# Performance work log

Measured on AMD Instinct MI355X. Metric: run time of the kernel, lower is better.

Reference implementation:

```python
import jax, jax.numpy as jnp
import numpy as np

N = 50000      # num nodes
E = 800000     # num edges (avg degree 16)
H = 128        # hidden_dim
D = 3          # node_dim (decoder output)
L = 4          # num_layers


def setup_inputs() -> dict:
    key = jax.random.key(0)
    ks = jax.random.split(key, 6)
    s = 0.05
    x = jax.random.normal(ks[0], (N, H), dtype=jnp.float32)
    edge_index = jax.random.randint(ks[1], (2, E), 0, N, dtype=jnp.int64)
    # per-layer EdgeConv MLP params: Linear(2H->H), ReLU, Linear(H->H)
    W1 = jax.random.normal(ks[2], (L, 2 * H, H), dtype=jnp.float32) * s
    b1 = jnp.zeros((L, H), dtype=jnp.float32)
    W2 = jax.random.normal(ks[3], (L, H, H), dtype=jnp.float32) * s
    b2 = jnp.zeros((L, H), dtype=jnp.float32)
    # final fc: Linear(H -> D)
    Wf = jax.random.normal(ks[4], (H, D), dtype=jnp.float32) * s
    bf = jnp.zeros((D,), dtype=jnp.float32)
    return {"x": x, "edge_index": edge_index, "W1": W1, "b1": b1,
            "W2": W2, "b2": b2, "Wf": Wf, "bf": bf}


def reference(x, edge_index, W1, b1, W2, b2, Wf, bf):
    n = x.shape[0]
    # add_self_loops: every node has at least one incoming message
    loops = jnp.arange(n, dtype=edge_index.dtype)
    src = jnp.concatenate([edge_index[0], loops])  # x_j source
    dst = jnp.concatenate([edge_index[1], loops])  # x_i target / aggregate index
    for l in range(W1.shape[0]):
        x_i = x[dst]                                   # [E+N, H] gather targets
        x_j = x[src]                                   # [E+N, H] gather sources
        msg = jnp.concatenate([x_i, x_j - x_i], axis=-1)   # [E+N, 2H]
        msg = jax.nn.relu(msg @ W1[l] + b1[l]) @ W2[l] + b2[l]  # edge MLP
        x = jax.ops.segment_max(msg, dst, num_segments=n)       # max aggregate
    return x @ Wf + bf  # [N, D]
```

## Files before the change

### kernel.cpp

```cpp
#include <hip/hip_runtime.h>
#include <hip/hip_fp16.h>

typedef _Float16 f16;
typedef _Float16 f16x8 __attribute__((ext_vector_type(8)));
typedef __fp16 hf16x2 __attribute__((ext_vector_type(2)));
typedef float f32x4 __attribute__((ext_vector_type(4)));
typedef float f32x2 __attribute__((ext_vector_type(2)));
typedef unsigned int u32;
typedef u32 u32x4 __attribute__((ext_vector_type(4)));

#define HDIM 128
#define LAYERS 4
#define TS 48
#define NEG_BIG (-3.0e38f)

static __device__ __forceinline__ f32x4 mfma16(f16x8 a, f16x8 b, f32x4 c) {
  return __builtin_amdgcn_mfma_f32_16x16x32_f16(a, b, c, 0, 0, 0);
}

static __device__ __forceinline__ void atomicMaxF(float* addr, float val) {
  if (val >= 0.f) atomicMax((int*)addr, __float_as_int(val));
  else            atomicMin((unsigned int*)addr, __float_as_uint(val));
}

static __device__ __forceinline__ f16x8 pack4(hf16x2 a, hf16x2 b, hf16x2 c, hf16x2 d) {
  u32x4 u = {__builtin_bit_cast(u32, a), __builtin_bit_cast(u32, b),
             __builtin_bit_cast(u32, c), __builtin_bit_cast(u32, d)};
  return __builtin_bit_cast(f16x8, u);
}

static __device__ __forceinline__ void split8(f32x4 a, f32x4 b, f16x8& hv, f16x8& lv) {
  hf16x2 h0 = __builtin_amdgcn_cvt_pkrtz(a.x, a.y);
  hf16x2 h1 = __builtin_amdgcn_cvt_pkrtz(a.z, a.w);
  hf16x2 h2 = __builtin_amdgcn_cvt_pkrtz(b.x, b.y);
  hf16x2 h3 = __builtin_amdgcn_cvt_pkrtz(b.z, b.w);
  hv = pack4(h0, h1, h2, h3);
  hf16x2 l0 = __builtin_amdgcn_cvt_pkrtz(a.x - (float)h0[0], a.y - (float)h0[1]);
  hf16x2 l1 = __builtin_amdgcn_cvt_pkrtz(a.z - (float)h1[0], a.w - (float)h1[1]);
  hf16x2 l2 = __builtin_amdgcn_cvt_pkrtz(b.x - (float)h2[0], b.y - (float)h2[1]);
  hf16x2 l3 = __builtin_amdgcn_cvt_pkrtz(b.z - (float)h3[0], b.w - (float)h3[1]);
  lv = pack4(l0, l1, l2, l3);
}

__global__ void gnn_hist(const int* __restrict__ ei, int* __restrict__ deg, int E) {
  int e = blockIdx.x * 256 + threadIdx.x;
  if (e < E) atomicAdd(&deg[ei[E + e]], 1);
}

__global__ void gnn_bsum(const int* __restrict__ deg, int* __restrict__ bsum, int N) {
  __shared__ int red[256];
  int v = blockIdx.x * 256 + threadIdx.x;
  red[threadIdx.x] = (v < N) ? (deg[v] + 1) : 0;
  __syncthreads();
  for (int d = 128; d; d >>= 1) {
    if (threadIdx.x < d) red[threadIdx.x] += red[threadIdx.x + d];
    __syncthreads();
  }
  if (threadIdx.x == 0) bsum[blockIdx.x] = red[0];
}

__global__ void gnn_bscan(const int* __restrict__ bsum, int* __restrict__ boffs,
                          int* __restrict__ offs, int nb, int N) {
  __shared__ int sh[256];
  int t = threadIdx.x;
  sh[t] = (t < nb) ? bsum[t] : 0;
  __syncthreads();
  for (int d = 1; d < 256; d <<= 1) {
    int add = (t >= d) ? sh[t - d] : 0;
    __syncthreads();
    sh[t] += add;
    __syncthreads();
  }
  boffs[t] = (t > 0) ? sh[t - 1] : 0;
  if (t == 255) offs[N] = sh[255];
}

__global__ void gnn_scan_fin(const int* __restrict__ deg, const int* __restrict__ boffs,
                             int* __restrict__ offs, int* __restrict__ cursor,
                             int* __restrict__ colsrc, int* __restrict__ nodeof, int N) {
  __shared__ int sh[256];
  int t = threadIdx.x;
  int v = blockIdx.x * 256 + t;
  int val = (v < N) ? (deg[v] + 1) : 0;
  sh[t] = val;
  __syncthreads();
  for (int d = 1; d < 256; d <<= 1) {
    int add = (t >= d) ? sh[t - d] : 0;
    __syncthreads();
    sh[t] += add;
    __syncthreads();
  }
  if (v < N) {
    int excl = boffs[blockIdx.x] + sh[t] - val;
    offs[v] = excl;
    cursor[v] = excl + 1;
    colsrc[excl] = v;
    int e = excl + val;
    for (int s = excl; s < e; s++) nodeof[s] = v;
  }
}

__global__ void gnn_scatter(const int* __restrict__ ei, int* __restrict__ cursor,
                            int* __restrict__ colsrc, int E) {
  int e = blockIdx.x * 256 + threadIdx.x;
  if (e < E) {
    int d = ei[E + e];
    int p = atomicAdd(&cursor[d], 1);
    colsrc[p] = ei[e];
  }
}

__global__ void gnn_biasprep(const float* __restrict__ W1, const float* __restrict__ b1,
                             const float* __restrict__ b2, const float* __restrict__ Wf,
                             const float* __restrict__ bf, float* __restrict__ cbias,
                             float* __restrict__ bfp) {
  int l = blockIdx.x, c = threadIdx.x;
  if (l < LAYERS) {
    float s = 0.f;
    if (l > 0) {
      const float* bp = b2 + (size_t)(l - 1) * HDIM;
      if (c < 128) {
        for (int k = 0; k < 128; k++)
          s += bp[k] * (W1[((size_t)l * 256 + k) * 128 + c] - W1[((size_t)l * 256 + 128 + k) * 128 + c]);
      } else {
        int cc = c - 128;
        for (int k = 0; k < 128; k++)
          s += bp[k] * W1[((size_t)l * 256 + 128 + k) * 128 + cc];
      }
    }
    float base = (c < 128) ? b1[(size_t)l * HDIM + c] : 0.f;
    cbias[l * 256 + c] = base + s;
  } else if (c < 3) {
    float s = bf[c];
    for (int k = 0; k < 128; k++) s += b2[3 * HDIM + k] * Wf[k * 3 + c];
    bfp[c] = s;
  }
}

__global__ void gnn_wprep1(const float* __restrict__ W1, f16* __restrict__ Wc) {
  int id = blockIdx.x * 256 + threadIdx.x;
  if (id >= LAYERS * 128 * 256) return;
  int col = id & 255, k = (id >> 8) & 127, l = id >> 15;
  float w;
  if (col < 128) w = W1[((size_t)l * 256 + k) * 128 + col] - W1[((size_t)l * 256 + 128 + k) * 128 + col];
  else           w = W1[((size_t)l * 256 + 128 + k) * 128 + (col - 128)];
  f16 hi = (f16)w;
  f16 lo = (f16)(w - (float)hi);
  int kk = k >> 5, quad = (k >> 3) & 3, j = k & 7;
  int ntile = col >> 4, lane = quad * 16 + (col & 15);
  size_t base = ((((size_t)l * 2 + 0) * 4 + kk) * 16 + ntile) * 512 + lane * 8 + j;
  Wc[base] = hi;
  Wc[base + (size_t)4 * 16 * 512] = lo;
}

__global__ void gnn_wprep2(const float* __restrict__ W2, f16* __restrict__ W2f) {
  int id = blockIdx.x * 256 + threadIdx.x;
  if (id >= LAYERS * 128 * 128) return;
  int n = id & 127, k = (id >> 7) & 127, l = id >> 14;
  float w = W2[((size_t)l * 128 + k) * 128 + n];
  f16 hi = (f16)w;
  f16 lo = (f16)(w - (float)hi);
  int kk = k >> 5, quad = (k >> 3) & 3, j = k & 7;
  int ntile = n >> 4, lane = quad * 16 + (n & 15);
  size_t base = ((((size_t)l * 2 + 0) * 4 + kk) * 8 + ntile) * 512 + lane * 8 + j;
  W2f[base] = hi;
  W2f[base + (size_t)4 * 8 * 512] = lo;
}

__global__ __launch_bounds__(256) void gnn_pq(const float* __restrict__ x,
    const f16* __restrict__ Wc, const float* __restrict__ cbias,
    float* __restrict__ P, float* __restrict__ Q, int N,
    const int* __restrict__ offs, int spb, float* __restrict__ xinit) {
  __shared__ __align__(16) f16 shA[2 * 4 * 4 * 64 * 8];
  int tid = threadIdx.x;
  int row0 = blockIdx.x * 64;
#pragma unroll
  for (int i = 0; i < 4; i++) {
    int p = i * 256 + tid;
    int row = p & 63, seg = p >> 6;
    f32x4 a = {}, b = {};
    int gr = row0 + row;
    if (gr < N) {
      const f32x4* xp = (const f32x4*)(x + (size_t)gr * HDIM + seg * 8);
      a = xp[0]; b = xp[1];
    }
    f16x8 hv, lv;
    split8(a, b, hv, lv);
    int kk = seg >> 2, quad = seg & 3, mt = row >> 4, m = row & 15;
    int lane = quad * 16 + m;
    int off = ((kk * 4 + mt) * 64 + lane) * 8;
    *(f16x8*)&shA[off] = hv;
    *(f16x8*)&shA[off + 4 * 4 * 64 * 8] = lv;
  }
  __syncthreads();
  int wave = tid >> 6, lane = tid & 63;
  int quad = lane >> 4, cl = lane & 15;
  f16x8 bw[2][4][4];
#pragma unroll
  for (int pl = 0; pl < 2; pl++)
#pragma unroll
    for (int nt = 0; nt < 4; nt++)
#pragma unroll
      for (int kk = 0; kk < 4; kk++) {
        int ntile = wave * 4 + nt;
        bw[pl][nt][kk] = *(const f16x8*)&Wc[(((size_t)(pl * 4 + kk) * 16 + ntile) * 64 + lane) * 8];
      }
#pragma unroll
  for (int mt = 0; mt < 4; mt++) {
    f32x4 acc[4] = {};
#pragma unroll
    for (int kk = 0; kk < 4; kk++) {
      f16x8 ah = *(const f16x8*)&shA[((kk * 4 + mt) * 64 + lane) * 8];
      f16x8 al = *(const f16x8*)&shA[(((4 + kk) * 4 + mt) * 64 + lane) * 8];
#pragma unroll
      for (int nt = 0; nt < 4; nt++) {
        acc[nt] = mfma16(ah, bw[0][nt][kk], acc[nt]);
        acc[nt] = mfma16(al, bw[0][nt][kk], acc[nt]);
        acc[nt] = mfma16(ah, bw[1][nt][kk], acc[nt]);
      }
    }
#pragma unroll
    for (int nt = 0; nt < 4; nt++) {
      int c = (wave * 4 + nt) * 16 + cl;
      float bb = cbias[c];
      float* dst = (c < HDIM) ? P : Q;
      int cc = c & 127;
#pragma unroll
      for (int i = 0; i < 4; i++) {
        int gr = row0 + mt * 16 + quad * 4 + i;
        if (gr < N) dst[(size_t)gr * HDIM + cc] = acc[nt][i] + bb;
      }
    }
  }
  if (tid < 64) {
    int v = row0 + tid;
    if (v < N) {
      int a = offs[v], b = offs[v + 1] - 1;
      if (a / spb != b / spb) {
        f32x4 ninf = {NEG_BIG, NEG_BIG, NEG_BIG, NEG_BIG};
        float* xr = xinit + (size_t)v * HDIM;
#pragma unroll
        for (int c = 0; c < HDIM; c += 4) *(f32x4*)(xr + c) = ninf;
      }
    }
  }
}

__global__ __launch_bounds__(256, 3) void gnn_edge4(
    const float* __restrict__ P, const float* __restrict__ Q,
    const int* __restrict__ offs, const int* __restrict__ colsrc,
    const int* __restrict__ nodeof, const f16* __restrict__ W2f,
    float* __restrict__ xout, int S, int spb) {
  __shared__ __align__(16) f16 shA[2 * 4 * 3 * 64 * 8];
  __shared__ __align__(16) float msg[TS * 132];
  __shared__ __align__(16) float stradV[2][128];
  __shared__ int stradN[2];
  int tid = threadIdx.x;
  int wave = tid >> 6, lane = tid & 63;
  int quad = lane >> 4, cl = lane & 15;
  f16x8 bw[2][2][4];
#pragma unroll
  for (int pl = 0; pl < 2; pl++)
#pragma unroll
    for (int nt = 0; nt < 2; nt++)
#pragma unroll
      for (int kk = 0; kk < 4; kk++)
        bw[pl][nt][kk] = *(const f16x8*)&W2f[(((size_t)(pl * 4 + kk) * 8 + (wave * 2 + nt)) * 64 + lane) * 8];
  int blk0 = blockIdx.x * spb;
  int blk1 = blk0 + spb; if (blk1 > S) blk1 = S;
  if (tid < 2) stradN[tid] = -1;
  int sl = tid >> 4, seg = tid & 15;
  int kkb = seg >> 2, qb = seg & 3;
  int laneF = qb * 16 + sl;
  int tc = 0;
  for (int t0 = blk0; t0 < blk1; t0 += TS, tc++) {
    int par = tc & 1, prv = par ^ 1;
    int tEnd = t0 + TS; if (tEnd > blk1) tEnd = blk1;
#pragma unroll
    for (int i = 0; i < 3; i++) {
      int slot = t0 + i * 16 + sl;
      int slc = (slot < S) ? slot : (S - 1);
      int src = colsrc[slc];
      int dst = nodeof[slc];
      const f32x4* qp = (const f32x4*)(Q + (size_t)src * HDIM + seg * 8);
      const f32x4* pp = (const f32x4*)(P + (size_t)dst * HDIM + seg * 8);
      f32x4 qa = qp[0], qb4 = qp[1], pa = pp[0], pb = pp[1];
      f32x4 sa, sb;
      sa.x = fmaxf(pa.x + qa.x, 0.f); sa.y = fmaxf(pa.y + qa.y, 0.f);
      sa.z = fmaxf(pa.z + qa.z, 0.f); sa.w = fmaxf(pa.w + qa.w, 0.f);
      sb.x = fmaxf(pb.x + qb4.x, 0.f); sb.y = fmaxf(pb.y + qb4.y, 0.f);
      sb.z = fmaxf(pb.z + qb4.z, 0.f); sb.w = fmaxf(pb.w + qb4.w, 0.f);
      f16x8 hv, lv;
      split8(sa, sb, hv, lv);
      int off = ((kkb * 3 + i) * 64 + laneF) * 8;
      *(f16x8*)&shA[off] = hv;
      *(f16x8*)&shA[off + 6144] = lv;
    }
    __syncthreads();
    if (tid == 0) stradN[par] = -1;
    f32x4 acc[3][2] = {};
#pragma unroll
    for (int kk = 0; kk < 4; kk++)
#pragma unroll
      for (int mt = 0; mt < 3; mt++) {
        int off = ((kk * 3 + mt) * 64 + lane) * 8;
        f16x8 ah = *(const f16x8*)&shA[off];
        f16x8 al = *(const f16x8*)&shA[off + 6144];
#pragma unroll
        for (int nt = 0; nt < 2; nt++) {
          acc[mt][nt] = mfma16(ah, bw[0][nt][kk], acc[mt][nt]);
          acc[mt][nt] = mfma16(al, bw[0][nt][kk], acc[mt][nt]);
          acc[mt][nt] = mfma16(ah, bw[1][nt][kk], acc[mt][nt]);
        }
      }
#pragma unroll
    for (int mt = 0; mt < 3; mt++)
#pragma unroll
      for (int nt = 0; nt < 2; nt++) {
        int col = wave * 32 + nt * 16 + cl;
#pragma unroll
        for (int i = 0; i < 4; i++) {
          int row = mt * 16 + quad * 4 + i;
          msg[row * 132 + col] = acc[mt][nt][i];
        }
      }
    __syncthreads();
    int vA = nodeof[t0];
    int vB = nodeof[tEnd - 1];
    int sNp = stradN[prv];
    int ngroups = (vB - vA + 1) << 5;
    for (int p = tid; p < ngroups; p += 256) {
      int v = vA + (p >> 5), c4 = (p & 31) << 2;
      int a = offs[v], b = offs[v + 1];
      int r0 = (a > t0 ? a : t0) - t0;
      int r1 = (b < tEnd ? b : tEnd) - t0;
      f32x4 m = {NEG_BIG, NEG_BIG, NEG_BIG, NEG_BIG};
      for (int r = r0; r < r1; r++) {
        f32x4 x = *(const f32x4*)&msg[r * 132 + c4];
        m.x = fmaxf(m.x, x.x); m.y = fmaxf(m.y, x.y);
        m.z = fmaxf(m.z, x.z); m.w = fmaxf(m.w, x.w);
      }
      if (v == sNp) {
        f32x4 sv = *(const f32x4*)&stradV[prv][c4];
        m.x = fmaxf(m.x, sv.x); m.y = fmaxf(m.y, sv.y);
        m.z = fmaxf(m.z, sv.z); m.w = fmaxf(m.w, sv.w);
      }
      if (b > tEnd && tEnd < blk1) {
        *(f32x4*)&stradV[par][c4] = m;
        if ((p & 31) == 0) stradN[par] = v;
      } else {
        float* dp = &xout[(size_t)v * HDIM + c4];
        if (a < blk0 || b > blk1) {
          atomicMaxF(dp + 0, m.x); atomicMaxF(dp + 1, m.y);
          atomicMaxF(dp + 2, m.z); atomicMaxF(dp + 3, m.w);
        } else {
          *(f32x4*)dp = m;
        }
      }
    }
  }
}

__global__ __launch_bounds__(256) void gnn_fc(const float* __restrict__ x,
    const float* __restrict__ Wf, const float* __restrict__ bfp,
    float* __restrict__ out, int N) {
  int wave = threadIdx.x >> 6, lane = threadIdx.x & 63;
  int wid = blockIdx.x * 4 + wave, nw = gridDim.x * 4;
  int k0 = lane * 2;
  float w00 = Wf[k0 * 3 + 0], w01 = Wf[k0 * 3 + 1], w02 = Wf[k0 * 3 + 2];
  float w10 = Wf[k0 * 3 + 3], w11 = Wf[k0 * 3 + 4], w12 = Wf[k0 * 3 + 5];
  float bf0 = bfp[0], bf1 = bfp[1], bf2 = bfp[2];
  for (int v = wid; v < N; v += nw) {
    f32x2 xx = *(const f32x2*)(x + (size_t)v * HDIM + k0);
    float d0 = xx.x * w00 + xx.y * w10;
    float d1 = xx.x * w01 + xx.y * w11;
    float d2 = xx.x * w02 + xx.y * w12;
#pragma unroll
    for (int s = 32; s; s >>= 1) {
      d0 += __shfl_xor(d0, s, 64);
      d1 += __shfl_xor(d1, s, 64);
      d2 += __shfl_xor(d2, s, 64);
    }
    if (lane == 0) {
      out[(size_t)v * 3 + 0] = d0 + bf0;
      out[(size_t)v * 3 + 1] = d1 + bf1;
      out[(size_t)v * 3 + 2] = d2 + bf2;
    }
  }
}

extern "C" void kernel_launch(void* const* d_in, const int* in_sizes, int n_in,
                              void* d_out, int out_size, void* d_ws, size_t ws_size,
                              hipStream_t stream) {
  const float* x_in = (const float*)d_in[0];
  const int*   ei   = (const int*)d_in[1];
  const float* W1   = (const float*)d_in[2];
  const float* b1   = (const float*)d_in[3];
  const float* W2   = (const float*)d_in[4];
  const float* b2   = (const float*)d_in[5];
  const float* Wf   = (const float*)d_in[6];
  const float* bfv  = (const float*)d_in[7];
  float* outp = (float*)d_out;
  int N = in_sizes[0] / HDIM;
  int E = in_sizes[1] / 2;
  int S = E + N;

  char* ws = (char*)d_ws;
  size_t o = 0;
  auto alloc = [&](size_t bytes) -> char* {
    char* p = ws + o;
    o += (bytes + 255) & ~(size_t)255;
    return p;
  };
  int*   deg    = (int*)alloc((size_t)N * 4);
  int*   offs   = (int*)alloc(((size_t)N + 1) * 4);
  int*   cursor = (int*)alloc((size_t)N * 4);
  int*   colsrc = (int*)alloc((size_t)S * 4);
  int*   nodeof = (int*)alloc((size_t)S * 4);
  int*   bsum   = (int*)alloc(256 * 4);
  int*   boffs  = (int*)alloc(256 * 4);
  float* cbias  = (float*)alloc((size_t)LAYERS * 256 * 4);
  float* bfp    = (float*)alloc(4 * 4);
  float* P      = (float*)alloc((size_t)N * HDIM * 4);
  float* Q      = (float*)alloc((size_t)N * HDIM * 4);
  float* xbuf   = (float*)alloc((size_t)N * HDIM * 4);
  f16*   Wc     = (f16*)alloc((size_t)LAYERS * 65536 * 2);
  f16*   W2f    = (f16*)alloc((size_t)LAYERS * 32768 * 2);
  (void)ws_size; (void)n_in; (void)out_size;

  int nb = (N + 255) / 256;
  hipMemsetAsync(deg, 0, (size_t)N * 4, stream);
  gnn_hist<<<(E + 255) / 256, 256, 0, stream>>>(ei, deg, E);
  gnn_bsum<<<nb, 256, 0, stream>>>(deg, bsum, N);
  gnn_bscan<<<1, 256, 0, stream>>>(bsum, boffs, offs, nb, N);
  gnn_scan_fin<<<nb, 256, 0, stream>>>(deg, boffs, offs, cursor, colsrc, nodeof, N);
  gnn_scatter<<<(E + 255) / 256, 256, 0, stream>>>(ei, cursor, colsrc, E);
  gnn_biasprep<<<LAYERS + 1, 256, 0, stream>>>(W1, b1, b2, Wf, bfv, cbias, bfp);
  gnn_wprep1<<<(LAYERS * 128 * 256 + 255) / 256, 256, 0, stream>>>(W1, Wc);
  gnn_wprep2<<<(LAYERS * 128 * 128 + 255) / 256, 256, 0, stream>>>(W2, W2f);

  int spb = ((((S + 1023) / 1024) + TS - 1) / TS) * TS;
  int NB = (S + spb - 1) / spb;
  const float* xc = x_in;
  for (int l = 0; l < LAYERS; l++) {
    gnn_pq<<<(N + 63) / 64, 256, 0, stream>>>(xc, Wc + (size_t)l * 65536, cbias + l * 256,
                                              P, Q, N, offs, spb, xbuf);
    gnn_edge4<<<NB, 256, 0, stream>>>(P, Q, offs, colsrc, nodeof, W2f + (size_t)l * 32768,
                                      xbuf, S, spb);
    xc = xbuf;
  }
  gnn_fc<<<256, 256, 0, stream>>>(xc, Wf, bfp, outp, N);
}
```

Before: 926.7 us.

## Software-prefetch next edge tile's P/Q gathers and shrink tile to 32

The edge kernel now loads the P/Q rows for the next tile into registers while the current tile's MFMA work runs, and prefetches colsrc/nodeof indices two tiles ahead. The tile size drops from 48 to 32 edge slots and occupancy is raised to 4 blocks per CU, which shrinks shared memory and accumulator use. The goal is to hide gather latency. In exchange, the extra prefetch registers raise register pressure, and the smaller tiles mean more loop iterations and barriers per slot.

```diff
diff --git a/kernel.cpp b/kernel.cpp
--- a/kernel.cpp
+++ b/kernel.cpp
@@ -11,7 +11,7 @@
 
 #define HDIM 128
 #define LAYERS 4
-#define TS 48
+#define TS 32
 #define NEG_BIG (-3.0e38f)
 
 static __device__ __forceinline__ f32x4 mfma16(f16x8 a, f16x8 b, f32x4 c) {
@@ -246,12 +246,12 @@
   }
 }
 
-__global__ __launch_bounds__(256, 3) void gnn_edge4(
+__global__ __launch_bounds__(256, 4) void gnn_edge5(
     const float* __restrict__ P, const float* __restrict__ Q,
     const int* __restrict__ offs, const int* __restrict__ colsrc,
     const int* __restrict__ nodeof, const f16* __restrict__ W2f,
     float* __restrict__ xout, int S, int spb) {
-  __shared__ __align__(16) f16 shA[2 * 4 * 3 * 64 * 8];
+  __shared__ __align__(16) f16 shA[2 * 4 * 2 * 64 * 8];
   __shared__ __align__(16) float msg[TS * 132];
   __shared__ __align__(16) float stradV[2][128];
   __shared__ int stradN[2];
@@ -272,40 +272,69 @@
   int sl = tid >> 4, seg = tid & 15;
   int kkb = seg >> 2, qb = seg & 3;
   int laneF = qb * 16 + sl;
+  int Sm1 = S - 1;
+
+  int cs[2], nd[2];
+  f32x4 qv[2][2], pv[2][2];
+#pragma unroll
+  for (int i = 0; i < 2; i++) {
+    int slc = blk0 + i * 16 + sl; slc = (slc < S) ? slc : Sm1;
+    cs[i] = colsrc[slc]; nd[i] = nodeof[slc];
+  }
+#pragma unroll
+  for (int i = 0; i < 2; i++) {
+    const f32x4* qp = (const f32x4*)(Q + (size_t)cs[i] * HDIM + seg * 8);
+    const f32x4* pp = (const f32x4*)(P + (size_t)nd[i] * HDIM + seg * 8);
+    qv[i][0] = qp[0]; qv[i][1] = qp[1];
+    pv[i][0] = pp[0]; pv[i][1] = pp[1];
+  }
+#pragma unroll
+  for (int i = 0; i < 2; i++) {
+    int slc = blk0 + TS + i * 16 + sl; slc = (slc < S) ? slc : Sm1;
+    cs[i] = colsrc[slc]; nd[i] = nodeof[slc];
+  }
+
   int tc = 0;
   for (int t0 = blk0; t0 < blk1; t0 += TS, tc++) {
     int par = tc & 1, prv = par ^ 1;
     int tEnd = t0 + TS; if (tEnd > blk1) tEnd = blk1;
 #pragma unroll
-    for (int i = 0; i < 3; i++) {
-      int slot = t0 + i * 16 + sl;
-      int slc = (slot < S) ? slot : (S - 1);
-      int src = colsrc[slc];
-      int dst = nodeof[slc];
-      const f32x4* qp = (const f32x4*)(Q + (size_t)src * HDIM + seg * 8);
-      const f32x4* pp = (const f32x4*)(P + (size_t)dst * HDIM + seg * 8);
-      f32x4 qa = qp[0], qb4 = qp[1], pa = pp[0], pb = pp[1];
+    for (int i = 0; i < 2; i++) {
       f32x4 sa, sb;
-      sa.x = fmaxf(pa.x + qa.x, 0.f); sa.y = fmaxf(pa.y + qa.y, 0.f);
-      sa.z = fmaxf(pa.z + qa.z, 0.f); sa.w = fmaxf(pa.w + qa.w, 0.f);
-      sb.x = fmaxf(pb.x + qb4.x, 0.f); sb.y = fmaxf(pb.y + qb4.y, 0.f);
-      sb.z = fmaxf(pb.z + qb4.z, 0.f); sb.w = fmaxf(pb.w + qb4.w, 0.f);
+      sa.x = fmaxf(pv[i][0].x + qv[i][0].x, 0.f); sa.y = fmaxf(pv[i][0].y + qv[i][0].y, 0.f);
+      sa.z = fmaxf(pv[i][0].z + qv[i][0].z, 0.f); sa.w = fmaxf(pv[i][0].w + qv[i][0].w, 0.f);
+      sb.x = fmaxf(pv[i][1].x + qv[i][1].x, 0.f); sb.y = fmaxf(pv[i][1].y + qv[i][1].y, 0.f);
+      sb.z = fmaxf(pv[i][1].z + qv[i][1].z, 0.f); sb.w = fmaxf(pv[i][1].w + qv[i][1].w, 0.f);
       f16x8 hv, lv;
       split8(sa, sb, hv, lv);
-      int off = ((kkb * 3 + i) * 64 + laneF) * 8;
+      int off = ((kkb * 2 + i) * 64 + laneF) * 8;
       *(f16x8*)&shA[off] = hv;
-      *(f16x8*)&shA[off + 6144] = lv;
+      *(f16x8*)&shA[off + 4096] = lv;
     }
     __syncthreads();
     if (tid == 0) stradN[par] = -1;
-    f32x4 acc[3][2] = {};
+    if (t0 + TS < blk1) {
+#pragma unroll
+      for (int i = 0; i < 2; i++) {
+        const f32x4* qp = (const f32x4*)(Q + (size_t)cs[i] * HDIM + seg * 8);
+        const f32x4* pp = (const f32x4*)(P + (size_t)nd[i] * HDIM + seg * 8);
+        qv[i][0] = qp[0]; qv[i][1] = qp[1];
+        pv[i][0] = pp[0]; pv[i][1] = pp[1];
+      }
+#pragma unroll
+      for (int i = 0; i < 2; i++) {
+        int slc = t0 + 2 * TS + i * 16 + sl; slc = (slc < S) ? slc : Sm1;
+        cs[i] = colsrc[slc]; nd[i] = nodeof[slc];
+      }
+    }
+    f32x4 acc[2][2] = {};
 #pragma unroll
     for (int kk = 0; kk < 4; kk++)
 #pragma unroll
-      for (int mt = 0; mt < 3; mt++) {
-        int off = ((kk * 3 + mt) * 64 + lane) * 8;
+      for (int mt = 0; mt < 2; mt++) {
+        int off = ((kk * 2 + mt) * 64 + lane) * 8;
         f16x8 ah = *(const f16x8*)&shA[off];
-        f16x8 al = *(const f16x8*)&shA[off + 6144];
+        f16x8 al = *(const f16x8*)&shA[off + 4096];
 #pragma unroll
         for (int nt = 0; nt < 2; nt++) {
           acc[mt][nt] = mfma16(ah, bw[0][nt][kk], acc[mt][nt]);
@@ -314,7 +343,7 @@
         }
       }
 #pragma unroll
-    for (int mt = 0; mt < 3; mt++)
+    for (int mt = 0; mt < 2; mt++)
 #pragma unroll
       for (int nt = 0; nt < 2; nt++) {
         int col = wave * 32 + nt * 16 + cl;
@@ -445,7 +474,7 @@
   for (int l = 0; l < LAYERS; l++) {
     gnn_pq<<<(N + 63) / 64, 256, 0, stream>>>(xc, Wc + (size_t)l * 65536, cbias + l * 256,
                                               P, Q, N, offs, spb, xbuf);
-    gnn_edge4<<<NB, 256, 0, stream>>>(P, Q, offs, colsrc, nodeof, W2f + (size_t)l * 32768,
+    gnn_edge5<<<NB, 256, 0, stream>>>(P, Q, offs, colsrc, nodeof, W2f + (size_t)l * 32768,
                                       xbuf, S, spb);
     xc = xbuf;
   }
```

After: 984.4 us. 1.06x slower.
